# Performance work log

Hardware: AMD Instinct MI355X
Metric: run time of the kernel (lower is better)

Reference implementation:

```python
import jax, jax.numpy as jnp
import numpy as np

HEADS = 12
LN_EPS = 1e-12
NUM_PROTOTYPES = 8


def _layer_norm(x, g, b):
    mu = x.mean(-1, keepdims=True)
    var = ((x - mu) ** 2).mean(-1, keepdims=True)
    return (x - mu) / jnp.sqrt(var + LN_EPS) * g + b


def _bert_attention(q_in, kv_in, wq, bq, wk, bk, wv, bv, wo, bo, ln_g, ln_b):
    # HF BertAttention: MHA (query from q_in, key/value from kv_in) then
    # SelfOutput: dense + residual(q_in) + LayerNorm. Dropout = 0 (eval).
    B, Sq, D = q_in.shape
    Sk = kv_in.shape[1]
    dh = D // HEADS
    q = (q_in @ wq + bq).reshape(B, Sq, HEADS, dh).transpose(0, 2, 1, 3)
    k = (kv_in @ wk + bk).reshape(B, Sk, HEADS, dh).transpose(0, 2, 1, 3)
    v = (kv_in @ wv + bv).reshape(B, Sk, HEADS, dh).transpose(0, 2, 1, 3)
    scores = jnp.einsum('bhqd,bhkd->bhqk', q, k) / jnp.sqrt(jnp.asarray(dh, q.dtype))
    probs = jax.nn.softmax(scores, axis=-1)
    ctx = jnp.einsum('bhqk,bhkd->bhqd', probs, v).transpose(0, 2, 1, 3).reshape(B, Sq, D)
    return _layer_norm(ctx @ wo + bo + q_in, ln_g, ln_b)


def setup_inputs() -> dict:
    key = jax.random.key(0)
    ks = jax.random.split(key, 16)
    D = 768
    inp = {
        'local_feats': jax.random.normal(ks[0], (8, 256, D), jnp.float32),
        'global_feat_dict': jax.random.normal(ks[1], (16384, D), jnp.float32),
    }
    i = 2
    for pre in ('ll', 'lg'):
        for nm in ('wq', 'wk', 'wv', 'wo'):
            inp[f'{pre}_{nm}'] = 0.02 * jax.random.normal(ks[i], (D, D), jnp.float32)
            i += 1
        for nm in ('bq', 'bk', 'bv', 'bo'):
            inp[f'{pre}_{nm}'] = jnp.zeros((D,), jnp.float32)
        inp[f'{pre}_ln_g'] = jnp.ones((D,), jnp.float32)
        inp[f'{pre}_ln_b'] = jnp.zeros((D,), jnp.float32)
    inp['ln_g'] = jnp.ones((D,), jnp.float32)
    inp['ln_b'] = jnp.zeros((D,), jnp.float32)
    inp['aug_w'] = 0.02 * jax.random.normal(ks[i], (D, 1), jnp.float32)
    inp['ori_w'] = 0.02 * jax.random.normal(ks[i + 1], (D, 1), jnp.float32)
    inp['aug_b'] = jnp.zeros((1,), jnp.float32)
    inp['ori_b'] = jnp.zeros((1,), jnp.float32)
    return inp


def reference(local_feats, global_feat_dict,
              ll_wq, ll_bq, ll_wk, ll_bk, ll_wv, ll_bv, ll_wo, ll_bo, ll_ln_g, ll_ln_b,
              lg_wq, lg_bq, lg_wk, lg_bk, lg_wv, lg_bv, lg_wo, lg_bo, lg_ln_g, lg_ln_b,
              ln_g, ln_b, aug_w, aug_b, ori_w, ori_b):
    B, L, D = local_feats.shape
    K = NUM_PROTOTYPES
    # similarity_topk retrieval: cosine similarity against prototype pool
    g_norm = global_feat_dict / jnp.linalg.norm(global_feat_dict, axis=-1, keepdims=True)
    t_norm = local_feats / jnp.linalg.norm(local_feats, axis=-1, keepdims=True)
    sim = jnp.einsum('bld,nd->bln', t_norm, g_norm)          # [B, L, N]
    topk_idx = jax.lax.top_k(sim, K)[1]                       # [B, L, K]
    global_feats = global_feat_dict[topk_idx].reshape(B, L * K, D)
    # self-attn over locals, cross-attn locals -> retrieved prototypes
    ll = _bert_attention(local_feats, local_feats,
                         ll_wq, ll_bq, ll_wk, ll_bk, ll_wv, ll_bv, ll_wo, ll_bo, ll_ln_g, ll_ln_b)
    lg = _bert_attention(local_feats, global_feats,
                         lg_wq, lg_bq, lg_wk, lg_bk, lg_wv, lg_bv, lg_wo, lg_bo, lg_ln_g, lg_ln_b)
    out = _layer_norm(ll + lg, ln_g, ln_b)
    aug_weight = jax.nn.sigmoid(out @ aug_w + aug_b + local_feats @ ori_w + ori_b)
    return aug_weight * out + (1.0 - aug_weight) * local_feats
```

## Files before the change

kernel.cpp:

```cpp
#include <hip/hip_runtime.h>
#include <math.h>

#define D     768
#define HEADS 12
#define DH    64
#define BATCH 8
#define LSEQ  256
#define MROWS 2048
#define NDICT 16384
#define TOPK  8

typedef _Float16 half_t;
typedef half_t half8 __attribute__((ext_vector_type(8)));
typedef half_t half4v __attribute__((ext_vector_type(4)));
typedef float floatx4 __attribute__((ext_vector_type(4)));

#define F_DICT   0u
#define F_TN     6291456u
#define F_LOC    7077888u
#define F_WT     7864320u
#define F_BF     10223616u
#define F_TOPI   10231808u
#define F_LP     10248192u
#define F_SIM    13393920u
#define F_CTX    30171136u
#define F_D1     30957568u
#define F_CANDV  30957568u
#define F_CANDI  31088640u
#define F_ML     34103296u
#define F_NRM    34299904u
#define F_USED   34316288u
#define F_ROWMAP 34332672u
#define F_INVMAP 34349056u
#define F_CNT    34365440u

typedef const __attribute__((address_space(1))) void* gptr_as1;
typedef __attribute__((address_space(3))) void* lptr_as3;
#define GLDS16(gp, lp) __builtin_amdgcn_global_load_lds((gptr_as1)(gp), (lptr_as3)(lp), 16, 0, 0)

__device__ __forceinline__ float wavesum(float s) {
#pragma unroll
  for (int d2 = 32; d2 > 0; d2 >>= 1) s += __shfl_xor(s, d2);
  return s;
}
__device__ __forceinline__ float bsum(float v, float* red) {
  int t = threadIdx.x;
  v = wavesum(v);
  if ((t & 63) == 0) red[t >> 6] = v;
  __syncthreads();
  float r = red[0] + red[1] + red[2] + red[3];
  __syncthreads();
  return r;
}

__global__ __launch_bounds__(256) void k_prep_wt(
    const float* __restrict__ dict, const float* __restrict__ local,
    half_t* __restrict__ gdict_h, float* __restrict__ dnrm,
    half_t* __restrict__ loc_h, half_t* __restrict__ tn_h,
    const float* w0, const float* w1, const float* w2, const float* w3,
    const float* w4, const float* w5, const float* w6, const float* w7,
    const float* b0, const float* b1, const float* b2, const float* b3,
    const float* b4, const float* b5, const float* b6, const float* b7,
    half_t* __restrict__ Wt, float* __restrict__ bfout) {
  __shared__ float tile[32][33];
  int g = blockIdx.x, t = threadIdx.x;
  int wid = t >> 6, lane = t & 63;
  if (g < 4096) {
    size_t r = (size_t)g * 4 + wid;
    const float4* xr = (const float4*)(dict + r * (size_t)D);
    float4 a = xr[lane], b = xr[lane + 64], c = xr[lane + 128];
    float s = a.x*a.x + a.y*a.y + a.z*a.z + a.w*a.w
            + b.x*b.x + b.y*b.y + b.z*b.z + b.w*b.w
            + c.x*c.x + c.y*c.y + c.z*c.z + c.w*c.w;
    s = wavesum(s);
    float n = sqrtf(s), inv = 1.0f / n;
    half4v* yr = (half4v*)(gdict_h + r * (size_t)D);
    half4v ha, hb, hc;
    ha[0]=(half_t)(a.x*inv); ha[1]=(half_t)(a.y*inv); ha[2]=(half_t)(a.z*inv); ha[3]=(half_t)(a.w*inv);
    hb[0]=(half_t)(b.x*inv); hb[1]=(half_t)(b.y*inv); hb[2]=(half_t)(b.z*inv); hb[3]=(half_t)(b.w*inv);
    hc[0]=(half_t)(c.x*inv); hc[1]=(half_t)(c.y*inv); hc[2]=(half_t)(c.z*inv); hc[3]=(half_t)(c.w*inv);
    yr[lane] = ha; yr[lane + 64] = hb; yr[lane + 128] = hc;
    if (lane == 0) dnrm[r] = n;
  } else if (g < 4608) {
    size_t r = (size_t)(g - 4096) * 4 + wid;
    const float4* xr = (const float4*)(local + r * (size_t)D);
    float4 a = xr[lane], b = xr[lane + 64], c = xr[lane + 128];
    float s = a.x*a.x + a.y*a.y + a.z*a.z + a.w*a.w
            + b.x*b.x + b.y*b.y + b.z*b.z + b.w*b.w
            + c.x*c.x + c.y*c.y + c.z*c.z + c.w*c.w;
    s = wavesum(s);
    float inv = 1.0f / sqrtf(s);
    half4v* rr = (half4v*)(loc_h + r * (size_t)D);
    half4v* nr = (half4v*)(tn_h + r * (size_t)D);
    half4v ra, rb, rc, na, nb, nc;
    ra[0]=(half_t)a.x; ra[1]=(half_t)a.y; ra[2]=(half_t)a.z; ra[3]=(half_t)a.w;
    rb[0]=(half_t)b.x; rb[1]=(half_t)b.y; rb[2]=(half_t)b.z; rb[3]=(half_t)b.w;
    rc[0]=(half_t)c.x; rc[1]=(half_t)c.y; rc[2]=(half_t)c.z; rc[3]=(half_t)c.w;
    na[0]=(half_t)(a.x*inv); na[1]=(half_t)(a.y*inv); na[2]=(half_t)(a.z*inv); na[3]=(half_t)(a.w*inv);
    nb[0]=(half_t)(b.x*inv); nb[1]=(half_t)(b.y*inv); nb[2]=(half_t)(b.z*inv); nb[3]=(half_t)(b.w*inv);
    nc[0]=(half_t)(c.x*inv); nc[1]=(half_t)(c.y*inv); nc[2]=(half_t)(c.z*inv); nc[3]=(half_t)(c.w*inv);
    rr[lane] = ra; rr[lane + 64] = rb; rr[lane + 128] = rc;
    nr[lane] = na; nr[lane + 64] = nb; nr[lane + 128] = nc;
  } else {
    const float* wsrcs[8] = {w0,w1,w2,w3,w4,w5,w6,w7};
    const float* bsrcs[8] = {b0,b1,b2,b3,b4,b5,b6,b7};
    int id = g - 4608;
    int z = id / 576, rem = id % 576;
    int by = rem / 24, bx = rem % 24;
    const float* Wsrc = wsrcs[z];
    half_t* dst = Wt + (size_t)z * D * D;
    int tx = t & 31, ty = t >> 5;
    int c0 = bx * 32, r0 = by * 32;
#pragma unroll
    for (int j = 0; j < 4; j++)
      tile[ty + j*8][tx] = Wsrc[(size_t)(r0 + ty + j*8) * D + c0 + tx];
    __syncthreads();
#pragma unroll
    for (int j = 0; j < 4; j++)
      dst[(size_t)(c0 + ty + j*8) * D + r0 + tx] = (half_t)tile[tx][ty + j*8];
    if (bx == 0 && by == 0) {
#pragma unroll
      for (int j = 0; j < 3; j++)
        bfout[z * D + t + j*256] = bsrcs[z][t + j*256];
    }
  }
}

__device__ __forceinline__ void hgemm_core(
    const half_t* __restrict__ A, const half_t* __restrict__ B,
    const float* __restrict__ bias, const float* __restrict__ dnrm,
    const int* __restrict__ rowmap, void* __restrict__ Cout,
    int N, int K, int outHalf, int bx, int by, int mhalf,
    half_t* As, half_t* Bs) {
  int tid = threadIdx.x;
  int wid = tid >> 6, lane = tid & 63;
  int l16 = lane & 15, quad = lane >> 4;
  int n0 = bx * 128, m0 = by * 128;
  if (mhalf && m0 >= mhalf) { B += (size_t)D * D; if (bias) bias += D; }
  int wm = (wid & 1) * 64, wn = (wid >> 1) * 64;

  int r0  = tid >> 3;
  int cbg = (tid & 7) ^ (r0 & 7);
  const half_t* Aps[4];
#pragma unroll
  for (int i = 0; i < 4; i++) {
    int mm = m0 + r0 + 32*i;
    int mr = rowmap ? rowmap[mm] : mm;
    Aps[i] = A + (size_t)mr * K + cbg * 8;
  }
  const half_t* Bp = B + (size_t)(n0 + r0) * K + cbg * 8;

  floatx4 acc[4][4];
#pragma unroll
  for (int i = 0; i < 4; i++)
#pragma unroll
    for (int j = 0; j < 4; j++) { acc[i][j][0]=0.f; acc[i][j][1]=0.f; acc[i][j][2]=0.f; acc[i][j][3]=0.f; }

  for (int k0 = 0; k0 < K; k0 += 64) {
#pragma unroll
    for (int i = 0; i < 4; i++)
      GLDS16(Aps[i] + k0, As + ((size_t)i*256 + wid*64) * 8);
#pragma unroll
    for (int i = 0; i < 4; i++)
      GLDS16(Bp + k0 + (size_t)i * 32 * K, Bs + ((size_t)i*256 + wid*64) * 8);
    __syncthreads();
#pragma unroll
    for (int ks = 0; ks < 2; ks++) {
      half8 af[4], bf[4];
#pragma unroll
      for (int i = 0; i < 4; i++) {
        int row = wm + i*16 + l16;
        int cb = (quad + ks*4) ^ (row & 7);
        af[i] = *(const half8*)&As[row*64 + cb*8];
      }
#pragma unroll
      for (int j = 0; j < 4; j++) {
        int row = wn + j*16 + l16;
        int cb = (quad + ks*4) ^ (row & 7);
        bf[j] = *(const half8*)&Bs[row*64 + cb*8];
      }
#pragma unroll
      for (int i = 0; i < 4; i++)
#pragma unroll
        for (int j = 0; j < 4; j++)
          acc[i][j] = __builtin_amdgcn_mfma_f32_16x16x32_f16(af[i], bf[j], acc[i][j], 0, 0, 0);
    }
    __syncthreads();
  }

  float bcol[4];
#pragma unroll
  for (int j = 0; j < 4; j++) bcol[j] = bias ? bias[n0 + wn + j*16 + l16] : 0.f;
  if (outHalf) {
    half_t* C = (half_t*)Cout;
#pragma unroll
    for (int i = 0; i < 4; i++)
#pragma unroll
      for (int r = 0; r < 4; r++) {
        int grow = m0 + wm + i*16 + quad*4 + r;
        float sc = dnrm ? dnrm[rowmap ? rowmap[grow] : grow] : 1.0f;
#pragma unroll
        for (int j = 0; j < 4; j++)
          C[(size_t)grow * N + n0 + wn + j*16 + l16] = (half_t)(acc[i][j][r] * sc + bcol[j]);
      }
  } else {
    float* C = (float*)Cout;
#pragma unroll
    for (int i = 0; i < 4; i++)
#pragma unroll
      for (int r = 0; r < 4; r++) {
        int grow = m0 + wm + i*16 + quad*4 + r;
        float sc = dnrm ? dnrm[rowmap ? rowmap[grow] : grow] : 1.0f;
#pragma unroll
        for (int j = 0; j < 4; j++)
          C[(size_t)grow * N + n0 + wn + j*16 + l16] = acc[i][j][r] * sc + bcol[j];
      }
  }
}

__device__ __forceinline__ void hgemm256_core(
    const half_t* __restrict__ A, const half_t* __restrict__ B,
    const float* __restrict__ bias, const float* __restrict__ dnrm,
    const int* __restrict__ rowmap, half_t* __restrict__ C,
    int N, int K, int bx, int by,
    half_t* As0, half_t* As1, half_t* Bs0, half_t* Bs1) {
  const int tid = threadIdx.x;
  const int wid = tid >> 6, lane = tid & 63;
  const int l16 = lane & 15, quad = lane >> 4;
  const int m0 = by * 256, n0 = bx * 256;

  const int r0 = tid >> 3;
  const int cg = (tid & 7) ^ (r0 & 7);
  const half_t* Aps[4]; const half_t* Bps[4];
#pragma unroll
  for (int i = 0; i < 4; i++) {
    int mm = m0 + r0 + i * 64;
    int mr = rowmap ? rowmap[mm] : mm;
    Aps[i] = A + (size_t)mr * K + cg * 8;
    Bps[i] = B + (size_t)(n0 + r0 + i * 64) * K + cg * 8;
  }

  const int arow = (wid & 3) * 32 + l16;
  const int brow = (wid >> 2) * 64 + l16;
  const int cb0 = (quad ^ (l16 & 7)) * 8;
  const int cb1 = ((quad + 4) ^ (l16 & 7)) * 8;

  floatx4 acc[4][2][4];
#pragma unroll
  for (int q = 0; q < 4; q++)
#pragma unroll
    for (int mi = 0; mi < 2; mi++)
#pragma unroll
      for (int ni = 0; ni < 4; ni++) {
        acc[q][mi][ni][0] = 0.f; acc[q][mi][ni][1] = 0.f;
        acc[q][mi][ni][2] = 0.f; acc[q][mi][ni][3] = 0.f;
      }
  half8 af[2][2], bf[4][2];

#define STAGE(Adst, Bdst, kn) { \
    GLDS16(Aps[0] + (kn), (Adst) + (0*512 + wid*64) * 8); \
    GLDS16(Aps[1] + (kn), (Adst) + (1*512 + wid*64) * 8); \
    GLDS16(Aps[2] + (kn), (Adst) + (2*512 + wid*64) * 8); \
    GLDS16(Aps[3] + (kn), (Adst) + (3*512 + wid*64) * 8); \
    GLDS16(Bps[0] + (kn), (Bdst) + (0*512 + wid*64) * 8); \
    GLDS16(Bps[1] + (kn), (Bdst) + (1*512 + wid*64) * 8); \
    GLDS16(Bps[2] + (kn), (Bdst) + (2*512 + wid*64) * 8); \
    GLDS16(Bps[3] + (kn), (Bdst) + (3*512 + wid*64) * 8); }
#define LDA(qm) { const int rb_ = (qm)*8192 + arow*64; \
    af[0][0] = *(const half8*)&Ar[rb_ + cb0];        af[0][1] = *(const half8*)&Ar[rb_ + cb1]; \
    af[1][0] = *(const half8*)&Ar[rb_ + 1024 + cb0]; af[1][1] = *(const half8*)&Ar[rb_ + 1024 + cb1]; }
#define LDB(qn) { const int rb_ = (qn)*8192 + brow*64; \
    bf[0][0] = *(const half8*)&Br[rb_ + cb0];        bf[0][1] = *(const half8*)&Br[rb_ + cb1]; \
    bf[1][0] = *(const half8*)&Br[rb_ + 1024 + cb0]; bf[1][1] = *(const half8*)&Br[rb_ + 1024 + cb1]; \
    bf[2][0] = *(const half8*)&Br[rb_ + 2048 + cb0]; bf[2][1] = *(const half8*)&Br[rb_ + 2048 + cb1]; \
    bf[3][0] = *(const half8*)&Br[rb_ + 3072 + cb0]; bf[3][1] = *(const half8*)&Br[rb_ + 3072 + cb1]; }
#define MM(q) { _Pragma("unroll") for (int mi = 0; mi < 2; mi++) { \
    _Pragma("unroll") for (int ni = 0; ni < 4; ni++) { \
      acc[q][mi][ni] = __builtin_amdgcn_mfma_f32_16x16x32_f16(af[mi][0], bf[ni][0], acc[q][mi][ni], 0, 0, 0); \
      acc[q][mi][ni] = __builtin_amdgcn_mfma_f32_16x16x32_f16(af[mi][1], bf[ni][1], acc[q][mi][ni], 0, 0, 0); } } }

  const int NT = K >> 6;
  STAGE(As0, Bs0, 0);
  __syncthreads();

  half_t* Ar = As0; half_t* Aw = As1;
  half_t* Br = Bs0; half_t* Bw = Bs1;
  for (int t = 0; t < NT; ++t) {
    if (t + 1 < NT) STAGE(Aw, Bw, (t + 1) * 64);
    LDA(0); LDB(0); MM(0);
    LDB(1);         MM(1);
    LDA(1);         MM(2);
    LDB(0);         MM(3);
    if (t + 1 < NT) __syncthreads();
    half_t* tp = Ar; Ar = Aw; Aw = tp;
    tp = Br; Br = Bw; Bw = tp;
  }

  float bcol[2][4];
#pragma unroll
  for (int qn = 0; qn < 2; qn++)
#pragma unroll
    for (int ni = 0; ni < 4; ni++)
      bcol[qn][ni] = bias ? bias[n0 + qn*128 + (wid >> 2)*64 + ni*16 + l16] : 0.f;
#pragma unroll
  for (int q = 0; q < 4; q++) {
    const int qm = q >> 1;
    const int qn = (q == 1 || q == 2) ? 1 : 0;
#pragma unroll
    for (int mi = 0; mi < 2; mi++)
#pragma unroll
      for (int r = 0; r < 4; r++) {
        int grow = m0 + qm*128 + (wid & 3)*32 + mi*16 + quad*4 + r;
        float sc = dnrm ? dnrm[rowmap ? rowmap[grow] : grow] : 1.0f;
#pragma unroll
        for (int ni = 0; ni < 4; ni++)
          C[(size_t)grow * N + n0 + qn*128 + (wid >> 2)*64 + ni*16 + l16] =
              (half_t)(acc[q][mi][ni][r] * sc + bcol[qn][ni]);
      }
  }
#undef STAGE
#undef LDA
#undef LDB
#undef MM
}

__global__ __launch_bounds__(512) void k_gemm_simlp(
    const half_t* __restrict__ tn, const half_t* __restrict__ gd,
    half_t* __restrict__ sim,
    const half_t* __restrict__ loc, const half_t* __restrict__ wt0,
    const float* __restrict__ bf0, half_t* __restrict__ lp) {
  __shared__ half_t As[2][256*64];
  __shared__ half_t Bs[2][256*64];
  int gid = blockIdx.x;
  int swz = (gid & 7) * 76 + (gid >> 3);
  if (swz < 512) {
    int bx = (swz & 7) + ((swz >> 3) >> 3) * 8;
    int by = (swz >> 3) & 7;
    hgemm256_core(tn, gd, nullptr, nullptr, nullptr, sim, NDICT, D, bx, by,
                  As[0], As[1], Bs[0], Bs[1]);
  } else {
    int rel = swz - 512;
    int bx = rel >> 3;
    int by = rel & 7;
    hgemm256_core(loc, wt0, bf0, nullptr, nullptr, lp, 3072, D, bx, by,
                  As[0], As[1], Bs[0], Bs[1]);
  }
}

__global__ __launch_bounds__(512) void k_gemm_dkv(
    const half_t* __restrict__ gd, const half_t* __restrict__ wt4,
    const float* __restrict__ bf4, const float* __restrict__ dnrm,
    const int* __restrict__ rowmap, const int* __restrict__ cnt,
    half_t* __restrict__ dkv) {
  __shared__ half_t As[2][256*64];
  __shared__ half_t Bs[2][256*64];
  int mceil = (*cnt + 255) & ~255;
  if ((int)blockIdx.y * 256 >= mceil) return;
  hgemm256_core(gd, wt4, bf4, dnrm, rowmap, dkv, 1536, D,
                blockIdx.x, blockIdx.y, As[0], As[1], Bs[0], Bs[1]);
}

__global__ __launch_bounds__(256) void k_gemm_wo(
    const half_t* __restrict__ ctx, const half_t* __restrict__ wt6,
    const float* __restrict__ bf6, float* __restrict__ dd) {
  __shared__ half_t As[128*64];
  __shared__ half_t Bs[128*64];
  hgemm_core(ctx, wt6, bf6, nullptr, nullptr, dd, D, D, 0, blockIdx.x, blockIdx.y, MROWS, As, Bs);
}

__global__ __launch_bounds__(256) void k_topk1(const half_t* __restrict__ sim,
                                               float* __restrict__ candv,
                                               int* __restrict__ candi,
                                               int* __restrict__ used,
                                               int* __restrict__ rowmap,
                                               int* __restrict__ cnt) {
  int t = threadIdx.x;
  if (t < 4) used[blockIdx.x * 4 + t] = 0;
  else if (t < 8) rowmap[blockIdx.x * 4 + t - 4] = 0;
  if (blockIdx.x == 0 && t == 8) *cnt = 0;

  int gw = blockIdx.x * 4 + (t >> 6);
  int lane = t & 63;
  int row = gw >> 3, seg = gw & 7;
  int cbase = seg * 2048;
  const half_t* p = sim + (size_t)row * NDICT + cbase;

  float v[32];
#pragma unroll
  for (int i = 0; i < 4; i++) {
    half8 h = *(const half8*)(p + i*512 + lane*8);
#pragma unroll
    for (int j = 0; j < 8; j++) v[i*8 + j] = (float)h[j];
  }
  float m = v[0]; int pos = 0;
#pragma unroll
  for (int i = 1; i < 32; i++) { if (v[i] > m) { m = v[i]; pos = i; } }

  for (int it = 0; it < 8; it++) {
    int gidx = cbase + (pos >> 3) * 512 + lane * 8 + (pos & 7);
    float bv = m; int bi = gidx;
#pragma unroll
    for (int d2 = 1; d2 < 64; d2 <<= 1) {
      float ov = __shfl_xor(bv, d2); int oi = __shfl_xor(bi, d2);
      if (ov > bv || (ov == bv && oi < bi)) { bv = ov; bi = oi; }
    }
    if (lane == 0) {
      size_t base = (size_t)row * 64 + seg * 8 + it;
      candv[base] = bv; candi[base] = bi;
    }
    if (bi == gidx) {
      v[pos] = -INFINITY;
      m = v[0]; pos = 0;
#pragma unroll
      for (int i = 1; i < 32; i++) { if (v[i] > m) { m = v[i]; pos = i; } }
    }
  }
}

__global__ __launch_bounds__(256) void k_topk2(const float* __restrict__ candv,
                                               const int* __restrict__ candi,
                                               int* __restrict__ topi,
                                               int* __restrict__ used) {
  int row = blockIdx.x * 4 + (threadIdx.x >> 6);
  int lane = threadIdx.x & 63;
  float v = candv[(size_t)row * 64 + lane];
  int id = candi[(size_t)row * 64 + lane];
#pragma unroll
  for (int it = 0; it < 8; it++) {
    float bv = v; int bi = id;
#pragma unroll
    for (int d2 = 1; d2 < 64; d2 <<= 1) {
      float ov = __shfl_xor(bv, d2); int oi = __shfl_xor(bi, d2);
      if (ov > bv || (ov == bv && oi < bi)) { bv = ov; bi = oi; }
    }
    if (lane == 0) { topi[row * 8 + it] = bi; used[bi] = 1; }
    if (id == bi) { v = -INFINITY; id = 0x7FFFFFFF; }
  }
}

__global__ __launch_bounds__(256) void k_cmp(const int* __restrict__ used,
                                             int* __restrict__ rowmap,
                                             int* __restrict__ invmap,
                                             int* __restrict__ cnt) {
  int i = blockIdx.x * 256 + threadIdx.x;
  if (used[i]) { int s = atomicAdd(cnt, 1); rowmap[s] = i; invmap[i] = s; }
}

__global__ __launch_bounds__(256) void k_flash2(
    const half_t* __restrict__ lp, const half_t* __restrict__ dkv,
    const int* __restrict__ topi_, const int* __restrict__ invmap,
    half_t* __restrict__ ctx_ll, half_t* __restrict__ Opart, float* __restrict__ ml) {
  __shared__ half_t Ks[64][72];
  __shared__ half_t Vt[64][72];
  __shared__ half_t Ps[4][16][72];

  int tid = threadIdx.x;
  int wid = tid >> 6;
  int lane = tid & 63;
  int l16 = lane & 15, quad = lane >> 4;

  const half_t *Q, *K, *V; const int* kidx; half_t* Out;
  int qS, kvS, Sk, ns, rel;
  if (blockIdx.x < BATCH*HEADS*4*4) {
    rel = blockIdx.x;
    Q = lp + 2304; qS = 3072; K = dkv; V = dkv + 768; kvS = 1536;
    kidx = topi_; Sk = LSEQ*TOPK; ns = 4; Out = nullptr;
  } else {
    rel = blockIdx.x - BATCH*HEADS*4*4;
    Q = lp; qS = 3072; K = lp + 768; V = lp + 1536; kvS = 3072;
    kidx = nullptr; Sk = LSEQ; ns = 1; Out = ctx_ll;
  }

  int sp = rel % ns;
  int rest = rel / ns;
  int qt = rest & 3;
  int h  = (rest >> 2) % HEADS;
  int bb = rest / (4 * HEADS);
  int q0 = qt * 64 + wid * 16;
  int sLen = Sk / ns, s0 = sp * sLen;

  const float SCL = 0.125f * 1.4426950408889634f;
  const half_t* qrow = Q + (size_t)(bb * LSEQ + q0 + l16) * qS + h * DH;
  half8 aq0 = *(const half8*)(qrow + quad*8);
  half8 aq1 = *(const half8*)(qrow + 32 + quad*8);

  floatx4 o[4];
#pragma unroll
  for (int nt = 0; nt < 4; nt++) { o[nt][0]=0.f; o[nt][1]=0.f; o[nt][2]=0.f; o[nt][3]=0.f; }
  float mreg[4] = {-INFINITY, -INFINITY, -INFINITY, -INFINITY};
  float lreg[4] = {0.f, 0.f, 0.f, 0.f};

  for (int k0 = s0; k0 < s0 + sLen; k0 += 64) {
    {
      int row = tid >> 2, cg = tid & 3;
      int key = k0 + row;
      size_t rowid = kidx ? (size_t)invmap[kidx[(size_t)bb * Sk + key]]
                          : (size_t)(bb * LSEQ + key);
      const half_t* kb = K + rowid * (size_t)kvS + h * DH + cg * 16;
      const half_t* vb = V + rowid * (size_t)kvS + h * DH + cg * 16;
      *(half8*)&Ks[row][cg*16]     = *(const half8*)kb;
      *(half8*)&Ks[row][cg*16 + 8] = *(const half8*)(kb + 8);
      half8 v0 = *(const half8*)vb, v1 = *(const half8*)(vb + 8);
#pragma unroll
      for (int jj = 0; jj < 8; jj++) { Vt[cg*16 + jj][row] = v0[jj]; Vt[cg*16 + 8 + jj][row] = v1[jj]; }
    }
    __syncthreads();

    floatx4 c[4];
#pragma unroll
    for (int nt = 0; nt < 4; nt++) {
      half8 b0 = *(const half8*)&Ks[nt*16 + l16][quad*8];
      half8 b1 = *(const half8*)&Ks[nt*16 + l16][32 + quad*8];
      floatx4 z; z[0]=0.f; z[1]=0.f; z[2]=0.f; z[3]=0.f;
      z = __builtin_amdgcn_mfma_f32_16x16x32_f16(aq0, b0, z, 0, 0, 0);
      z = __builtin_amdgcn_mfma_f32_16x16x32_f16(aq1, b1, z, 0, 0, 0);
      c[nt] = z;
    }

    float alpha[4];
#pragma unroll
    for (int r = 0; r < 4; r++) {
      float mx = fmaxf(fmaxf(c[0][r], c[1][r]), fmaxf(c[2][r], c[3][r]));
      mx = fmaxf(mx, __shfl_xor(mx, 1));
      mx = fmaxf(mx, __shfl_xor(mx, 2));
      mx = fmaxf(mx, __shfl_xor(mx, 4));
      mx = fmaxf(mx, __shfl_xor(mx, 8));
      float mn = fmaxf(mreg[r], mx);
      float al = __builtin_amdgcn_exp2f((mreg[r] - mn) * SCL);
      float ps = 0.f;
#pragma unroll
      for (int nt = 0; nt < 4; nt++) {
        float p = __builtin_amdgcn_exp2f((c[nt][r] - mn) * SCL);
        c[nt][r] = p; ps += p;
      }
      ps += __shfl_xor(ps, 1);
      ps += __shfl_xor(ps, 2);
      ps += __shfl_xor(ps, 4);
      ps += __shfl_xor(ps, 8);
      mreg[r] = mn; lreg[r] = lreg[r] * al + ps; alpha[r] = al;
    }

#pragma unroll
    for (int nt = 0; nt < 4; nt++)
#pragma unroll
      for (int r = 0; r < 4; r++)
        Ps[wid][quad*4 + r][nt*16 + l16] = (half_t)c[nt][r];
    half8 p0 = *(const half8*)&Ps[wid][l16][quad*8];
    half8 p1 = *(const half8*)&Ps[wid][l16][32 + quad*8];

#pragma unroll
    for (int nt = 0; nt < 4; nt++)
#pragma unroll
      for (int r = 0; r < 4; r++) o[nt][r] *= alpha[r];
#pragma unroll
    for (int nt = 0; nt < 4; nt++) {
      half8 v0 = *(const half8*)&Vt[nt*16 + l16][quad*8];
      half8 v1 = *(const half8*)&Vt[nt*16 + l16][32 + quad*8];
      o[nt] = __builtin_amdgcn_mfma_f32_16x16x32_f16(p0, v0, o[nt], 0, 0, 0);
      o[nt] = __builtin_amdgcn_mfma_f32_16x16x32_f16(p1, v1, o[nt], 0, 0, 0);
    }
    __syncthreads();
  }

  if (ns == 1) {
    half_t* ob = Out + (size_t)(bb * LSEQ + q0 + quad*4) * D + h * DH;
#pragma unroll
    for (int r = 0; r < 4; r++) {
      float inv = 1.0f / lreg[r];
#pragma unroll
      for (int nt = 0; nt < 4; nt++)
        ob[(size_t)r * D + nt*16 + l16] = (half_t)(o[nt][r] * inv);
    }
  } else {
    size_t rbase = (size_t)sp * MROWS + bb * LSEQ + q0 + quad*4;
    half_t* ob = Opart + rbase * D + h * DH;
#pragma unroll
    for (int r = 0; r < 4; r++) {
      float inv = 1.0f / lreg[r];
#pragma unroll
      for (int nt = 0; nt < 4; nt++)
        ob[(size_t)r * D + nt*16 + l16] = (half_t)(o[nt][r] * inv);
    }
    if (l16 == 0) {
#pragma unroll
      for (int r = 0; r < 4; r++) {
        size_t mi = ((rbase + r) * HEADS + h) * 2;
        ml[mi] = mreg[r]; ml[mi + 1] = lreg[r];
      }
    }
  }
}

__global__ __launch_bounds__(256) void k_comb(const half_t* __restrict__ Op,
                                              const float* __restrict__ ml,
                                              half_t* __restrict__ ctx) {
  int r = blockIdx.x, t = threadIdx.x;
  const float SCL = 0.125f * 1.4426950408889634f;
#pragma unroll
  for (int i = 0; i < 3; i++) {
    int col = t + i*256;
    int h = col >> 6;
    float m[4], l[4];
    float ms = -INFINITY;
#pragma unroll
    for (int s = 0; s < 4; s++) {
      size_t mi = (((size_t)s * MROWS + r) * HEADS + h) * 2;
      m[s] = ml[mi]; l[s] = ml[mi + 1];
      ms = fmaxf(ms, m[s]);
    }
    float den = 0.f, num = 0.f;
#pragma unroll
    for (int s = 0; s < 4; s++) {
      float w = __builtin_amdgcn_exp2f((m[s] - ms) * SCL) * l[s];
      den += w;
      num += w * (float)Op[((size_t)s * MROWS + r) * D + col];
    }
    ctx[(size_t)r * D + col] = (half_t)(num / den);
  }
}

__global__ __launch_bounds__(256) void k_lngate3(
    const float* __restrict__ dd, const float* __restrict__ loc,
    const float* __restrict__ llg, const float* __restrict__ llb,
    const float* __restrict__ lgg, const float* __restrict__ lgb,
    const float* __restrict__ lng, const float* __restrict__ lnb,
    const float* __restrict__ aw, const float* __restrict__ ow,
    const float* __restrict__ ab, const float* __restrict__ orb,
    float* __restrict__ y) {
  __shared__ float red[8];
  size_t r = blockIdx.x; int t = threadIdx.x;
  const float* ar = dd + r*(size_t)D;
  const float* br = dd + ((size_t)MROWS + r)*(size_t)D;
  const float* lcl = loc + r*(size_t)D;
  float l0 = lcl[t], l1 = lcl[t+256], l2 = lcl[t+512];

  float a0 = ar[t]+l0, a1 = ar[t+256]+l1, a2 = ar[t+512]+l2;
  float mu = bsum(a0+a1+a2, red) * (1.0f/768.0f);
  float d0 = a0-mu, d1 = a1-mu, d2 = a2-mu;
  float var = bsum(d0*d0 + d1*d1 + d2*d2, red) * (1.0f/768.0f);
  float rstd = rsqrtf(var + 1e-12f);
  float x0 = d0*rstd*llg[t]     + llb[t];
  float x1 = d1*rstd*llg[t+256] + llb[t+256];
  float x2 = d2*rstd*llg[t+512] + llb[t+512];

  float b0 = br[t]+l0, b1 = br[t+256]+l1, b2 = br[t+512]+l2;
  mu = bsum(b0+b1+b2, red) * (1.0f/768.0f);
  d0 = b0-mu; d1 = b1-mu; d2 = b2-mu;
  var = bsum(d0*d0 + d1*d1 + d2*d2, red) * (1.0f/768.0f);
  rstd = rsqrtf(var + 1e-12f);
  x0 += d0*rstd*lgg[t]     + lgb[t];
  x1 += d1*rstd*lgg[t+256] + lgb[t+256];
  x2 += d2*rstd*lgg[t+512] + lgb[t+512];

  mu = bsum(x0+x1+x2, red) * (1.0f/768.0f);
  d0 = x0-mu; d1 = x1-mu; d2 = x2-mu;
  var = bsum(d0*d0 + d1*d1 + d2*d2, red) * (1.0f/768.0f);
  rstd = rsqrtf(var + 1e-12f);
  float o0 = d0*rstd*lng[t]     + lnb[t];
  float o1 = d1*rstd*lng[t+256] + lnb[t+256];
  float o2 = d2*rstd*lng[t+512] + lnb[t+512];

  float s = o0*aw[t] + l0*ow[t]
          + o1*aw[t+256] + l1*ow[t+256]
          + o2*aw[t+512] + l2*ow[t+512];
  float z = bsum(s, red) + ab[0] + orb[0];
  float w = 1.0f / (1.0f + __expf(-z));
  float* yr = y + r*(size_t)D;
  yr[t]     = w*o0 + (1.f-w)*l0;
  yr[t+256] = w*o1 + (1.f-w)*l1;
  yr[t+512] = w*o2 + (1.f-w)*l2;
}

extern "C" void kernel_launch(void* const* d_in, const int* in_sizes, int n_in,
                              void* d_out, int out_size, void* d_ws, size_t ws_size,
                              hipStream_t stream) {
  (void)in_sizes; (void)n_in; (void)out_size; (void)ws_size;
  const float* local = (const float*)d_in[0];
  const float* dict  = (const float*)d_in[1];
  const float* ll_g  = (const float*)d_in[10];
  const float* ll_b  = (const float*)d_in[11];
  const float* lg_g  = (const float*)d_in[20];
  const float* lg_b  = (const float*)d_in[21];
  const float* ln_g  = (const float*)d_in[22];
  const float* ln_b  = (const float*)d_in[23];
  const float* aug_w = (const float*)d_in[24];
  const float* ori_w = (const float*)d_in[25];
  const float* aug_b = (const float*)d_in[26];
  const float* ori_b = (const float*)d_in[27];

  float* W = (float*)d_ws;
  half_t* gdict_h = (half_t*)(W + F_DICT);
  half_t* tn_h    = (half_t*)(W + F_TN);
  half_t* loc_h   = (half_t*)(W + F_LOC);
  half_t* wt      = (half_t*)(W + F_WT);
  float*  bf      = W + F_BF;
  int*    topi    = (int*)(W + F_TOPI);
  half_t* lp      = (half_t*)(W + F_LP);
  half_t* sim_h   = (half_t*)(W + F_SIM);
  half_t* dkv     = (half_t*)(W + F_SIM);
  float*  dd      = W + F_SIM;
  half_t* ctx_ll  = (half_t*)(W + F_CTX);
  half_t* ctx_lg  = (half_t*)(W + F_D1);
  half_t* Opart   = (half_t*)(W + F_D1);
  float*  candv   = W + F_CANDV;
  int*    candi   = (int*)(W + F_CANDI);
  float*  ml      = W + F_ML;
  float*  dnrm    = W + F_NRM;
  int*    used    = (int*)(W + F_USED);
  int*    rowmap  = (int*)(W + F_ROWMAP);
  int*    invmap  = (int*)(W + F_INVMAP);
  int*    cnt     = (int*)(W + F_CNT);

  dim3 blk(256);
  dim3 blk5(512);
  const size_t WS = (size_t)D * D;

  k_prep_wt<<<4096 + 512 + 4608, blk, 0, stream>>>(
      dict, local, gdict_h, dnrm, loc_h, tn_h,
      (const float*)d_in[2], (const float*)d_in[3], (const float*)d_in[4],
      (const float*)d_in[12], (const float*)d_in[13], (const float*)d_in[14],
      (const float*)d_in[5], (const float*)d_in[15],
      (const float*)d_in[6], (const float*)d_in[7], (const float*)d_in[8],
      (const float*)d_in[16], (const float*)d_in[17], (const float*)d_in[18],
      (const float*)d_in[9], (const float*)d_in[19], wt, bf);

  k_gemm_simlp<<<512 + 96, blk5, 0, stream>>>(tn_h, gdict_h, sim_h,
                                              loc_h, wt + 0*WS, bf + 0, lp);

  k_topk1<<<MROWS*8/4, blk, 0, stream>>>(sim_h, candv, candi, used, rowmap, cnt);
  k_topk2<<<MROWS/4, blk, 0, stream>>>(candv, candi, topi, used);
  k_cmp<<<64, blk, 0, stream>>>(used, rowmap, invmap, cnt);

  k_gemm_dkv<<<dim3(6, 64), blk5, 0, stream>>>(
      gdict_h, wt + 4*WS, bf + 3072, dnrm, rowmap, cnt, dkv);

  k_flash2<<<dim3(BATCH*HEADS*4*4 + BATCH*HEADS*4), blk, 0, stream>>>(
      lp, dkv, topi, invmap, ctx_ll, Opart, ml);
  k_comb<<<MROWS, blk, 0, stream>>>(Opart, ml, ctx_lg);

  k_gemm_wo<<<dim3(6, 32), blk, 0, stream>>>(ctx_ll, wt + 6*WS, bf + 4608, dd);

  k_lngate3<<<MROWS, blk, 0, stream>>>(dd, local,
      ll_g, ll_b, lg_g, lg_b, ln_g, ln_b,
      aug_w, ori_w, aug_b, ori_b, (float*)d_out);
}
```

Baseline: 421.7 us.

## Interleave quarter-tile global-to-LDS staging with MFMA phases in 256 hgemm core

Replaces the simple double-buffered loop (stage whole next tile, compute, full __syncthreads) with a finer-grained schedule. Each A/B quarter is staged into LDS as soon as the compute phase that last read it has passed a barrier, with explicit vmcnt waits and raw s_barrier plus sched_barrier. The aim is to spread global loads across the compute phases and avoid draining all memory traffic at every tile boundary. It adds many more barriers and relies on careful buffer-reuse ordering. It also assumes NT is even and at least 2.

New measurement: 426.6 us. No clear change (+1.2%).

```diff
diff --git a/kernel.cpp b/kernel.cpp
--- a/kernel.cpp
+++ b/kernel.cpp
@@ -257,43 +257,81 @@
       }
   half8 af[2][2], bf[4][2];
 
-#define STAGE(Adst, Bdst, kn) { \
-    GLDS16(Aps[0] + (kn), (Adst) + (0*512 + wid*64) * 8); \
-    GLDS16(Aps[1] + (kn), (Adst) + (1*512 + wid*64) * 8); \
-    GLDS16(Aps[2] + (kn), (Adst) + (2*512 + wid*64) * 8); \
-    GLDS16(Aps[3] + (kn), (Adst) + (3*512 + wid*64) * 8); \
-    GLDS16(Bps[0] + (kn), (Bdst) + (0*512 + wid*64) * 8); \
-    GLDS16(Bps[1] + (kn), (Bdst) + (1*512 + wid*64) * 8); \
-    GLDS16(Bps[2] + (kn), (Bdst) + (2*512 + wid*64) * 8); \
-    GLDS16(Bps[3] + (kn), (Bdst) + (3*512 + wid*64) * 8); }
-#define LDA(qm) { const int rb_ = (qm)*8192 + arow*64; \
-    af[0][0] = *(const half8*)&Ar[rb_ + cb0];        af[0][1] = *(const half8*)&Ar[rb_ + cb1]; \
-    af[1][0] = *(const half8*)&Ar[rb_ + 1024 + cb0]; af[1][1] = *(const half8*)&Ar[rb_ + 1024 + cb1]; }
-#define LDB(qn) { const int rb_ = (qn)*8192 + brow*64; \
-    bf[0][0] = *(const half8*)&Br[rb_ + cb0];        bf[0][1] = *(const half8*)&Br[rb_ + cb1]; \
-    bf[1][0] = *(const half8*)&Br[rb_ + 1024 + cb0]; bf[1][1] = *(const half8*)&Br[rb_ + 1024 + cb1]; \
-    bf[2][0] = *(const half8*)&Br[rb_ + 2048 + cb0]; bf[2][1] = *(const half8*)&Br[rb_ + 2048 + cb1]; \
-    bf[3][0] = *(const half8*)&Br[rb_ + 3072 + cb0]; bf[3][1] = *(const half8*)&Br[rb_ + 3072 + cb1]; }
+#define STG_A(dst, i, kn) GLDS16(Aps[i] + (kn), (dst) + ((i)*512 + wid*64) * 8)
+#define STG_B(dst, i, kn) GLDS16(Bps[i] + (kn), (dst) + ((i)*512 + wid*64) * 8)
+#define LDA(buf, qm) { const int rb_ = (qm)*8192 + arow*64; \
+    af[0][0] = *(const half8*)&buf[rb_ + cb0];        af[0][1] = *(const half8*)&buf[rb_ + cb1]; \
+    af[1][0] = *(const half8*)&buf[rb_ + 1024 + cb0]; af[1][1] = *(const half8*)&buf[rb_ + 1024 + cb1]; }
+#define LDB(buf, qn) { const int rb_ = (qn)*8192 + brow*64; \
+    bf[0][0] = *(const half8*)&buf[rb_ + cb0];        bf[0][1] = *(const half8*)&buf[rb_ + cb1]; \
+    bf[1][0] = *(const half8*)&buf[rb_ + 1024 + cb0]; bf[1][1] = *(const half8*)&buf[rb_ + 1024 + cb1]; \
+    bf[2][0] = *(const half8*)&buf[rb_ + 2048 + cb0]; bf[2][1] = *(const half8*)&buf[rb_ + 2048 + cb1]; \
+    bf[3][0] = *(const half8*)&buf[rb_ + 3072 + cb0]; bf[3][1] = *(const half8*)&buf[rb_ + 3072 + cb1]; }
 #define MM(q) { _Pragma("unroll") for (int mi = 0; mi < 2; mi++) { \
     _Pragma("unroll") for (int ni = 0; ni < 4; ni++) { \
       acc[q][mi][ni] = __builtin_amdgcn_mfma_f32_16x16x32_f16(af[mi][0], bf[ni][0], acc[q][mi][ni], 0, 0, 0); \
       acc[q][mi][ni] = __builtin_amdgcn_mfma_f32_16x16x32_f16(af[mi][1], bf[ni][1], acc[q][mi][ni], 0, 0, 0); } } }
+#define VMC(n) asm volatile("s_waitcnt vmcnt(" #n ")" ::: "memory")
+#define SBAR() { __builtin_amdgcn_s_barrier(); __builtin_amdgcn_sched_barrier(0); }
 
   const int NT = K >> 6;
-  STAGE(As0, Bs0, 0);
-  __syncthreads();
-
-  half_t* Ar = As0; half_t* Aw = As1;
-  half_t* Br = Bs0; half_t* Bw = Bs1;
-  for (int t = 0; t < NT; ++t) {
-    if (t + 1 < NT) STAGE(Aw, Bw, (t + 1) * 64);
-    LDA(0); LDB(0); MM(0);
-    LDB(1);         MM(1);
-    LDA(1);         MM(2);
-    LDB(0);         MM(3);
-    if (t + 1 < NT) __syncthreads();
-    half_t* tp = Ar; Ar = Aw; Aw = tp;
-    tp = Br; Br = Bw; Bw = tp;
+  const int NIT = (NT >> 1) - 1;
+
+  STG_A(As0, 0, 0);  STG_A(As0, 1, 0);
+  STG_B(Bs0, 2, 0);  STG_B(Bs0, 3, 0);
+  STG_A(As0, 2, 0);  STG_A(As0, 3, 0);
+  STG_B(Bs0, 0, 0);  STG_B(Bs0, 1, 0);
+  STG_A(As1, 0, 64); STG_A(As1, 1, 64);
+  STG_B(Bs1, 2, 64); STG_B(Bs1, 3, 64);
+  VMC(4); SBAR();
+
+  for (int i = 0; i < NIT; ++i) {
+    const int k1 = (2*i+1)*64, k2 = (2*i+2)*64, k3 = (2*i+3)*64;
+    STG_A(As1, 2, k1); STG_A(As1, 3, k1);
+    LDA(As0, 0); LDB(Bs0, 0); MM(0);
+    SBAR();
+    STG_B(Bs1, 0, k1); STG_B(Bs1, 1, k1);
+    LDB(Bs0, 1); MM(1);
+    SBAR();
+    STG_A(As0, 0, k2); STG_A(As0, 1, k2);
+    LDA(As0, 1); MM(2);
+    SBAR();
+    STG_B(Bs0, 2, k2); STG_B(Bs0, 3, k2);
+    LDB(Bs0, 0); MM(3);
+    VMC(4); SBAR();
+    STG_A(As0, 2, k2); STG_A(As0, 3, k2);
+    LDA(As1, 0); LDB(Bs1, 0); MM(0);
+    SBAR();
+    STG_B(Bs0, 0, k2); STG_B(Bs0, 1, k2);
+    LDB(Bs1, 1); MM(1);
+    SBAR();
+    STG_A(As1, 0, k3); STG_A(As1, 1, k3);
+    LDA(As1, 1); MM(2);
+    SBAR();
+    STG_B(Bs1, 2, k3); STG_B(Bs1, 3, k3);
+    LDB(Bs1, 0); MM(3);
+    VMC(4); SBAR();
+  }
+
+  {
+    const int kL = (NT - 1) * 64;
+    STG_A(As1, 2, kL); STG_A(As1, 3, kL);
+    LDA(As0, 0); LDB(Bs0, 0); MM(0);
+    SBAR();
+    STG_B(Bs1, 0, kL); STG_B(Bs1, 1, kL);
+    LDB(Bs0, 1); MM(1);
+    SBAR();
+    LDA(As0, 1); MM(2);
+    SBAR();
+    LDB(Bs0, 0); MM(3);
+    VMC(0); SBAR();
+    LDA(As1, 0); LDB(Bs1, 0); MM(0);
+    SBAR();
+    LDB(Bs1, 1); MM(1);
+    SBAR();
+    LDA(As1, 1); MM(2);
+    SBAR();
+    LDB(Bs1, 0); MM(3);
   }
 
   float bcol[2][4];
@@ -318,10 +356,13 @@
               (half_t)(acc[q][mi][ni][r] * sc + bcol[qn][ni]);
       }
   }
-#undef STAGE
+#undef STG_A
+#undef STG_B
 #undef LDA
 #undef LDB
 #undef MM
+#undef VMC
+#undef SBAR
 }
 
 __global__ __launch_bounds__(512) void k_gemm_simlp(
```

## Fuse per-tile top-k selection into similarity GEMM epilogue, drop sim matrix

Applied to the files above, without the earlier changes.

The similarity GEMM no longer writes the 2048x16384 fp16 similarity matrix. Each 256x256 tile is staged in LDS, and every row extracts its top-8 candidates from the tile in place. A single merge kernel then reduces the 64 tiles x 8 candidates per row, and the used/rowmap/cnt reset moves into the prep kernel. This removes roughly 64MB of global write and re-read, at the cost of a serial per-row selection loop inside the GEMM epilogue.

Result: slower. 823.8 us (+95.4%).

```diff
diff --git a/kernel.cpp b/kernel.cpp
--- a/kernel.cpp
+++ b/kernel.cpp
@@ -26,7 +26,7 @@
 #define F_CTX    30171136u
 #define F_D1     30957568u
 #define F_CANDV  30957568u
-#define F_CANDI  31088640u
+#define F_CANDI  32006144u
 #define F_ML     34103296u
 #define F_NRM    34299904u
 #define F_USED   34316288u
@@ -61,11 +61,17 @@
     const float* w4, const float* w5, const float* w6, const float* w7,
     const float* b0, const float* b1, const float* b2, const float* b3,
     const float* b4, const float* b5, const float* b6, const float* b7,
-    half_t* __restrict__ Wt, float* __restrict__ bfout) {
+    half_t* __restrict__ Wt, float* __restrict__ bfout,
+    int* __restrict__ used, int* __restrict__ rowmap, int* __restrict__ cnt) {
   __shared__ float tile[32][33];
   int g = blockIdx.x, t = threadIdx.x;
   int wid = t >> 6, lane = t & 63;
   if (g < 4096) {
+    if (g < 64) {
+      used[(g << 8) | t] = 0;
+      rowmap[(g << 8) | t] = 0;
+      if (g == 0 && t == 0) *cnt = 0;
+    }
     size_t r = (size_t)g * 4 + wid;
     const float4* xr = (const float4*)(dict + r * (size_t)D);
     float4 a = xr[lane], b = xr[lane + 64], c = xr[lane + 128];
@@ -222,12 +228,16 @@
     const half_t* __restrict__ A, const half_t* __restrict__ B,
     const float* __restrict__ bias, const float* __restrict__ dnrm,
     const int* __restrict__ rowmap, half_t* __restrict__ C,
-    int N, int K, int bx, int by,
-    half_t* As0, half_t* As1, half_t* Bs0, half_t* Bs1) {
+    float* __restrict__ candv, int* __restrict__ candi,
+    int N, int K, int bx, int by, half_t* S) {
   const int tid = threadIdx.x;
   const int wid = tid >> 6, lane = tid & 63;
   const int l16 = lane & 15, quad = lane >> 4;
   const int m0 = by * 256, n0 = bx * 256;
+  half_t* As0 = S;
+  half_t* As1 = S + 16384;
+  half_t* Bs0 = S + 32768;
+  half_t* Bs1 = S + 49152;
 
   const int r0 = tid >> 3;
   const int cg = (tid & 7) ^ (r0 & 7);
@@ -296,27 +306,75 @@
     tp = Br; Br = Bw; Bw = tp;
   }
 
-  float bcol[2][4];
-#pragma unroll
-  for (int qn = 0; qn < 2; qn++)
-#pragma unroll
-    for (int ni = 0; ni < 4; ni++)
-      bcol[qn][ni] = bias ? bias[n0 + qn*128 + (wid >> 2)*64 + ni*16 + l16] : 0.f;
-#pragma unroll
-  for (int q = 0; q < 4; q++) {
-    const int qm = q >> 1;
-    const int qn = (q == 1 || q == 2) ? 1 : 0;
-#pragma unroll
-    for (int mi = 0; mi < 2; mi++)
-#pragma unroll
-      for (int r = 0; r < 4; r++) {
-        int grow = m0 + qm*128 + (wid & 3)*32 + mi*16 + quad*4 + r;
-        float sc = dnrm ? dnrm[rowmap ? rowmap[grow] : grow] : 1.0f;
-#pragma unroll
-        for (int ni = 0; ni < 4; ni++)
-          C[(size_t)grow * N + n0 + qn*128 + (wid >> 2)*64 + ni*16 + l16] =
-              (half_t)(acc[q][mi][ni][r] * sc + bcol[qn][ni]);
+  if (candv) {
+    __syncthreads();
+    half_t* tile = S;
+#pragma unroll
+    for (int q = 0; q < 4; q++) {
+      const int qm = q >> 1;
+      const int qn = (q == 1 || q == 2) ? 1 : 0;
+#pragma unroll
+      for (int mi = 0; mi < 2; mi++)
+#pragma unroll
+        for (int r = 0; r < 4; r++) {
+          int lrow = qm*128 + (wid & 3)*32 + mi*16 + quad*4 + r;
+#pragma unroll
+          for (int ni = 0; ni < 4; ni++)
+            tile[lrow*256 + qn*128 + (wid >> 2)*64 + ni*16 + l16] =
+                (half_t)acc[q][mi][ni][r];
+        }
+    }
+    __syncthreads();
+    for (int rr = 0; rr < 32; ++rr) {
+      int lrow = wid*32 + rr;
+      half4v hv = *(const half4v*)&tile[lrow*256 + lane*4];
+      float f[4];
+#pragma unroll
+      for (int j = 0; j < 4; j++) f[j] = (float)hv[j];
+      float m = f[0]; int pos = 0;
+#pragma unroll
+      for (int j = 1; j < 4; j++) { if (f[j] > m) { m = f[j]; pos = j; } }
+      size_t obase = (size_t)(m0 + lrow) * 512 + (size_t)bx * 8;
+      for (int it = 0; it < 8; ++it) {
+        int gi = n0 + lane*4 + pos;
+        float bv = m; int bi = gi;
+#pragma unroll
+        for (int d2 = 1; d2 < 64; d2 <<= 1) {
+          float ov = __shfl_xor(bv, d2); int oi = __shfl_xor(bi, d2);
+          if (ov > bv || (ov == bv && oi < bi)) { bv = ov; bi = oi; }
+        }
+        if (lane == 0) { candv[obase + it] = bv; candi[obase + it] = bi; }
+        if (bi == gi) {
+          f[pos] = -INFINITY;
+          m = f[0]; pos = 0;
+#pragma unroll
+          for (int j = 1; j < 4; j++) { if (f[j] > m) { m = f[j]; pos = j; } }
+        }
       }
+    }
+  } else {
+    float bcol[2][4];
+#pragma unroll
+    for (int qn = 0; qn < 2; qn++)
+#pragma unroll
+      for (int ni = 0; ni < 4; ni++)
+        bcol[qn][ni] = bias ? bias[n0 + qn*128 + (wid >> 2)*64 + ni*16 + l16] : 0.f;
+#pragma unroll
+    for (int q = 0; q < 4; q++) {
+      const int qm = q >> 1;
+      const int qn = (q == 1 || q == 2) ? 1 : 0;
+#pragma unroll
+      for (int mi = 0; mi < 2; mi++)
+#pragma unroll
+        for (int r = 0; r < 4; r++) {
+          int grow = m0 + qm*128 + (wid & 3)*32 + mi*16 + quad*4 + r;
+          float sc = dnrm ? dnrm[rowmap ? rowmap[grow] : grow] : 1.0f;
+#pragma unroll
+          for (int ni = 0; ni < 4; ni++)
+            C[(size_t)grow * N + n0 + qn*128 + (wid >> 2)*64 + ni*16 + l16] =
+                (half_t)(acc[q][mi][ni][r] * sc + bcol[qn][ni]);
+        }
+    }
   }
 #undef STAGE
 #undef LDA
@@ -326,24 +384,23 @@
 
 __global__ __launch_bounds__(512) void k_gemm_simlp(
     const half_t* __restrict__ tn, const half_t* __restrict__ gd,
-    half_t* __restrict__ sim,
+    float* __restrict__ candv, int* __restrict__ candi,
     const half_t* __restrict__ loc, const half_t* __restrict__ wt0,
     const float* __restrict__ bf0, half_t* __restrict__ lp) {
-  __shared__ half_t As[2][256*64];
-  __shared__ half_t Bs[2][256*64];
+  __shared__ half_t S[4 * 16384];
   int gid = blockIdx.x;
   int swz = (gid & 7) * 76 + (gid >> 3);
   if (swz < 512) {
     int bx = (swz & 7) + ((swz >> 3) >> 3) * 8;
     int by = (swz >> 3) & 7;
-    hgemm256_core(tn, gd, nullptr, nullptr, nullptr, sim, NDICT, D, bx, by,
-                  As[0], As[1], Bs[0], Bs[1]);
+    hgemm256_core(tn, gd, nullptr, nullptr, nullptr, nullptr, candv, candi,
+                  NDICT, D, bx, by, S);
   } else {
     int rel = swz - 512;
     int bx = rel >> 3;
     int by = rel & 7;
-    hgemm256_core(loc, wt0, bf0, nullptr, nullptr, lp, 3072, D, bx, by,
-                  As[0], As[1], Bs[0], Bs[1]);
+    hgemm256_core(loc, wt0, bf0, nullptr, nullptr, lp, nullptr, nullptr,
+                  3072, D, bx, by, S);
   }
 }
 
@@ -352,12 +409,11 @@
     const float* __restrict__ bf4, const float* __restrict__ dnrm,
     const int* __restrict__ rowmap, const int* __restrict__ cnt,
     half_t* __restrict__ dkv) {
-  __shared__ half_t As[2][256*64];
-  __shared__ half_t Bs[2][256*64];
+  __shared__ half_t S[4 * 16384];
   int mceil = (*cnt + 255) & ~255;
   if ((int)blockIdx.y * 256 >= mceil) return;
-  hgemm256_core(gd, wt4, bf4, dnrm, rowmap, dkv, 1536, D,
-                blockIdx.x, blockIdx.y, As[0], As[1], Bs[0], Bs[1]);
+  hgemm256_core(gd, wt4, bf4, dnrm, rowmap, dkv, nullptr, nullptr,
+                1536, D, blockIdx.x, blockIdx.y, S);
 }
 
 __global__ __launch_bounds__(256) void k_gemm_wo(
@@ -368,73 +424,37 @@
   hgemm_core(ctx, wt6, bf6, nullptr, nullptr, dd, D, D, 0, blockIdx.x, blockIdx.y, MROWS, As, Bs);
 }
 
-__global__ __launch_bounds__(256) void k_topk1(const half_t* __restrict__ sim,
-                                               float* __restrict__ candv,
-                                               int* __restrict__ candi,
-                                               int* __restrict__ used,
-                                               int* __restrict__ rowmap,
-                                               int* __restrict__ cnt) {
-  int t = threadIdx.x;
-  if (t < 4) used[blockIdx.x * 4 + t] = 0;
-  else if (t < 8) rowmap[blockIdx.x * 4 + t - 4] = 0;
-  if (blockIdx.x == 0 && t == 8) *cnt = 0;
-
-  int gw = blockIdx.x * 4 + (t >> 6);
-  int lane = t & 63;
-  int row = gw >> 3, seg = gw & 7;
-  int cbase = seg * 2048;
-  const half_t* p = sim + (size_t)row * NDICT + cbase;
-
-  float v[32];
-#pragma unroll
-  for (int i = 0; i < 4; i++) {
-    half8 h = *(const half8*)(p + i*512 + lane*8);
-#pragma unroll
-    for (int j = 0; j < 8; j++) v[i*8 + j] = (float)h[j];
-  }
-  float m = v[0]; int pos = 0;
-#pragma unroll
-  for (int i = 1; i < 32; i++) { if (v[i] > m) { m = v[i]; pos = i; } }
-
-  for (int it = 0; it < 8; it++) {
-    int gidx = cbase + (pos >> 3) * 512 + lane * 8 + (pos & 7);
-    float bv = m; int bi = gidx;
-#pragma unroll
-    for (int d2 = 1; d2 < 64; d2 <<= 1) {
-      float ov = __shfl_xor(bv, d2); int oi = __shfl_xor(bi, d2);
-      if (ov > bv || (ov == bv && oi < bi)) { bv = ov; bi = oi; }
-    }
-    if (lane == 0) {
-      size_t base = (size_t)row * 64 + seg * 8 + it;
-      candv[base] = bv; candi[base] = bi;
-    }
-    if (bi == gidx) {
-      v[pos] = -INFINITY;
-      m = v[0]; pos = 0;
-#pragma unroll
-      for (int i = 1; i < 32; i++) { if (v[i] > m) { m = v[i]; pos = i; } }
-    }
-  }
-}
-
-__global__ __launch_bounds__(256) void k_topk2(const float* __restrict__ candv,
+__global__ __launch_bounds__(256) void k_topkm(const float* __restrict__ candv,
                                                const int* __restrict__ candi,
                                                int* __restrict__ topi,
                                                int* __restrict__ used) {
   int row = blockIdx.x * 4 + (threadIdx.x >> 6);
   int lane = threadIdx.x & 63;
-  float v = candv[(size_t)row * 64 + lane];
-  int id = candi[(size_t)row * 64 + lane];
-#pragma unroll
-  for (int it = 0; it < 8; it++) {
-    float bv = v; int bi = id;
+  float v[8]; int id[8];
+#pragma unroll
+  for (int j = 0; j < 8; j++) {
+    v[j]  = candv[(size_t)row * 512 + lane + 64*j];
+    id[j] = candi[(size_t)row * 512 + lane + 64*j];
+  }
+  float m = v[0]; int mid = id[0]; int pos = 0;
+#pragma unroll
+  for (int j = 1; j < 8; j++)
+    if (v[j] > m || (v[j] == m && id[j] < mid)) { m = v[j]; mid = id[j]; pos = j; }
+  for (int it = 0; it < 8; ++it) {
+    float bv = m; int bi = mid;
 #pragma unroll
     for (int d2 = 1; d2 < 64; d2 <<= 1) {
       float ov = __shfl_xor(bv, d2); int oi = __shfl_xor(bi, d2);
       if (ov > bv || (ov == bv && oi < bi)) { bv = ov; bi = oi; }
     }
     if (lane == 0) { topi[row * 8 + it] = bi; used[bi] = 1; }
-    if (id == bi) { v = -INFINITY; id = 0x7FFFFFFF; }
+    if (bi == mid) {
+      v[pos] = -INFINITY;
+      m = v[0]; mid = id[0]; pos = 0;
+#pragma unroll
+      for (int j = 1; j < 8; j++)
+        if (v[j] > m || (v[j] == m && id[j] < mid)) { m = v[j]; mid = id[j]; pos = j; }
+    }
   }
 }
 
@@ -696,7 +716,6 @@
   float*  bf      = W + F_BF;
   int*    topi    = (int*)(W + F_TOPI);
   half_t* lp      = (half_t*)(W + F_LP);
-  half_t* sim_h   = (half_t*)(W + F_SIM);
   half_t* dkv     = (half_t*)(W + F_SIM);
   float*  dd      = W + F_SIM;
   half_t* ctx_ll  = (half_t*)(W + F_CTX);
@@ -722,13 +741,13 @@
       (const float*)d_in[5], (const float*)d_in[15],
       (const float*)d_in[6], (const float*)d_in[7], (const float*)d_in[8],
       (const float*)d_in[16], (const float*)d_in[17], (const float*)d_in[18],
-      (const float*)d_in[9], (const float*)d_in[19], wt, bf);
-
-  k_gemm_simlp<<<512 + 96, blk5, 0, stream>>>(tn_h, gdict_h, sim_h,
+      (const float*)d_in[9], (const float*)d_in[19], wt, bf,
+      used, rowmap, cnt);
+
+  k_gemm_simlp<<<512 + 96, blk5, 0, stream>>>(tn_h, gdict_h, candv, candi,
                                               loc_h, wt + 0*WS, bf + 0, lp);
 
-  k_topk1<<<MROWS*8/4, blk, 0, stream>>>(sim_h, candv, candi, used, rowmap, cnt);
-  k_topk2<<<MROWS/4, blk, 0, stream>>>(candv, candi, topi, used);
+  k_topkm<<<MROWS/4, blk, 0, stream>>>(candv, candi, topi, used);
   k_cmp<<<64, blk, 0, stream>>>(used, rowmap, invmap, cnt);
 
   k_gemm_dkv<<<dim3(6, 64), blk5, 0, stream>>>(
```
